# Kernel optimization log

Measured on AMD Instinct MI355X. Metric: run time of the kernel, lower is better.

The kernel has to match this reference:

```python
import jax, jax.numpy as jnp
import numpy as np

N_NODES = 100000
N_EDGES = 1600000
IN_DIM = 33
HID = 128
N_CLASSES = 10
N_GRAPHS = 128


def _glorot(key, shape):
    fan_in, fan_out = shape[0], shape[1]
    lim = (6.0 / (fan_in + fan_out)) ** 0.5
    return jax.random.uniform(key, shape, jnp.float32, -lim, lim)


def setup_inputs() -> dict:
    key = jax.random.key(0)
    ks = jax.random.split(key, 20)
    x = jax.random.normal(ks[0], (N_NODES, IN_DIM), jnp.float32)
    edge_index = jax.random.randint(ks[1], (2, N_EDGES), 0, N_NODES, jnp.int64)
    edge_w = jax.random.uniform(ks[2], (N_EDGES,), jnp.float32)
    batch = jnp.sort(jax.random.randint(ks[3], (N_NODES,), 0, N_GRAPHS, jnp.int64))
    p = {
        "We": _glorot(ks[4], (IN_DIM, HID)), "be": jnp.zeros((HID,), jnp.float32),
        "W1": _glorot(ks[5], (HID, HID)), "b1": jnp.zeros((HID,), jnp.float32),
        "W2": _glorot(ks[6], (HID, HID)), "b2": jnp.zeros((HID,), jnp.float32),
        "W3": _glorot(ks[7], (HID, HID)), "b3": jnp.zeros((HID,), jnp.float32),
        "W4": _glorot(ks[8], (HID, HID)), "b4": jnp.zeros((HID,), jnp.float32),
        "Wr1": _glorot(ks[9], (HID, HID // 2)), "br1": jnp.zeros((HID // 2,), jnp.float32),
        "Wr2": _glorot(ks[10], (HID // 2, HID // 4)), "br2": jnp.zeros((HID // 4,), jnp.float32),
        "Wr3": _glorot(ks[11], (HID // 4, N_CLASSES)),
    }
    return dict(x=x, edge_index=edge_index, edge_w=edge_w, batch=batch, **p)


def reference(x, edge_index, edge_w, batch,
              We, be, W1, b1, W2, b2, W3, b3, W4, b4,
              Wr1, br1, Wr2, br2, Wr3):
    N = x.shape[0]
    row, col = edge_index[0], edge_index[1]
    # PyG gcn_norm with add_self_loops=True: append (i,i) edges with weight 1
    loop = jnp.arange(N)
    row2 = jnp.concatenate([row, loop])
    col2 = jnp.concatenate([col, loop])
    w2 = jnp.concatenate([edge_w, jnp.ones((N,), edge_w.dtype)])
    deg = jax.ops.segment_sum(w2, col2, num_segments=N)  # in-degree incl. self-loop
    dinv = jnp.where(deg > 0, deg ** -0.5, 0.0)
    norm = dinv[row2] * w2 * dinv[col2]  # [E+N] symmetric normalization

    def conv(h, W, b):
        h = h @ W  # linear transform first (PyG GCNConv)
        msg = norm[:, None] * h[row2]  # gather + scale
        return jax.ops.segment_sum(msg, col2, num_segments=N) + b  # scatter-add to targets

    h = x @ We + be
    h = jax.nn.relu(conv(h, W1, b1))
    h = jax.nn.relu(conv(h, W2, b2))
    h = jax.nn.relu(conv(h, W3, b3))
    h = jax.nn.relu(conv(h, W4, b4))

    # global mean pool over graphs
    sums = jax.ops.segment_sum(h, batch, num_segments=N_GRAPHS)
    cnt = jax.ops.segment_sum(jnp.ones((N,), h.dtype), batch, num_segments=N_GRAPHS)
    pooled = sums / jnp.maximum(cnt, 1.0)[:, None]  # [G, HID]

    r = jax.nn.relu(pooled @ Wr1 + br1)
    r = jax.nn.relu(r @ Wr2 + br2)
    return r @ Wr3  # [G, n_classes]
```

## Files before the change

### kernel.cpp

```cpp
#include <hip/hip_runtime.h>
#include <hip/hip_bf16.h>

#define NN 100000
#define NE 1600000
#define IN_DIM 33
#define HID 128
#define NG 128
#define NCLS 10

using short8 = __attribute__((ext_vector_type(8))) short;
using floatx4 = __attribute__((ext_vector_type(4))) float;

static __device__ __forceinline__ size_t szmul(int a, int b) {
    return (size_t)a * (size_t)b;
}

static __device__ __forceinline__ unsigned short f2bf(float f) {
    unsigned u = __float_as_uint(f);
    u += 0x7fffu + ((u >> 16) & 1u);
    return (unsigned short)(u >> 16);
}
static __device__ __forceinline__ float bf_lo(unsigned u) { return __uint_as_float(u << 16); }
static __device__ __forceinline__ float bf_hi(unsigned u) { return __uint_as_float(u & 0xffff0000u); }

__global__ void k_init(int* bucket_cnt, int* bucket_fill, float* gsum) {
    int i = blockIdx.x * blockDim.x + threadIdx.x;
    if (i < 513) { bucket_cnt[i] = 0; bucket_fill[i] = 0; }
    if (i < NG * HID) gsum[i] = 0.0f;
}


__global__ __launch_bounds__(256) void k_bhist(const int* __restrict__ col,
                                               int* __restrict__ bucket_cnt, int e, int nbk) {
    __shared__ int hist[512];
    int tid = threadIdx.x;
    for (int i = tid; i < nbk; i += 256) hist[i] = 0;
    __syncthreads();
    for (int i = blockIdx.x * 256 + tid; i < e; i += 256 * 256)
        atomicAdd(&hist[col[i] >> 8], 1);
    __syncthreads();
    for (int i = tid; i < nbk; i += 256)
        if (hist[i]) atomicAdd(&bucket_cnt[i], hist[i]);
}

__global__ void k_scan_small(int* data, int nb) {
    __shared__ int s[512];
    int t = threadIdx.x;
    int v = (t < nb) ? data[t] : 0;
    s[t] = v;
    __syncthreads();
    for (int o = 1; o < 512; o <<= 1) {
        int a = (t >= o) ? s[t - o] : 0;
        __syncthreads();
        s[t] += a;
        __syncthreads();
    }
    if (t < nb) data[t] = s[t] - v;
    if (t == nb - 1) data[nb] = s[t];
}

__global__ __launch_bounds__(256) void k_bin_scatter(const int* __restrict__ row,
                                                     const int* __restrict__ col,
                                                     const float* __restrict__ w,
                                                     const int* __restrict__ bucket_base,
                                                     int* __restrict__ bucket_fill,
                                                     uint2* __restrict__ binned, int e, int nbk) {
    __shared__ int hist[512], rnk[512], basub[512];
    int tid = threadIdx.x;
    int c0 = blockIdx.x * 2048;
    for (int i = tid; i < nbk; i += 256) { hist[i] = 0; rnk[i] = 0; }
    __syncthreads();
    int myb[8]; unsigned myp[8]; unsigned myw[8];
#pragma unroll
    for (int u = 0; u < 8; ++u) {
        int idx = c0 + u * 256 + tid;
        int b = -1;
        if (idx < e) {
            int c = col[idx];
            int r = row[idx];
            myw[u] = __float_as_uint(w[idx]);
            b = c >> 8;
            myp[u] = ((unsigned)(c & 255) << 17) | (unsigned)r;
            atomicAdd(&hist[b], 1);
        }
        myb[u] = b;
    }
    __syncthreads();
    for (int i = tid; i < nbk; i += 256) {
        int c = hist[i];
        basub[i] = (c > 0) ? (bucket_base[i] + atomicAdd(&bucket_fill[i], c)) : 0;
    }
    __syncthreads();
#pragma unroll
    for (int u = 0; u < 8; ++u) {
        int b = myb[u];
        if (b >= 0) {
            int rk = atomicAdd(&rnk[b], 1);
            binned[basub[b] + rk] = make_uint2(myp[u], myw[u]);
        }
    }
}

__global__ __launch_bounds__(256) void k_bucket_cnt(const uint2* __restrict__ binned,
                                                    const int* __restrict__ bucket_base,
                                                    int* __restrict__ cnt, int n) {
    __shared__ int c256[256];
    int b = blockIdx.x, tid = threadIdx.x;
    c256[tid] = 0;
    __syncthreads();
    int beg = bucket_base[b], end = bucket_base[b + 1];
    for (int e2 = beg + tid; e2 < end; e2 += 256)
        atomicAdd(&c256[(binned[e2].x >> 17) & 255], 1);
    __syncthreads();
    int node = b * 256 + tid;
    if (node < n) cnt[node] = c256[tid];
}

#define SCAN_B 1024
__global__ void k_scan1(const int* __restrict__ cnt, int* __restrict__ rowptr,
                        int* __restrict__ bsums, int n) {
    __shared__ int s[SCAN_B];
    int t = threadIdx.x;
    int i = blockIdx.x * SCAN_B + t;
    int v = (i < n) ? cnt[i] : 0;
    s[t] = v;
    __syncthreads();
    for (int o = 1; o < SCAN_B; o <<= 1) {
        int a = (t >= o) ? s[t - o] : 0;
        __syncthreads();
        s[t] += a;
        __syncthreads();
    }
    if (i < n) rowptr[i] = s[t] - v;
    if (t == SCAN_B - 1) bsums[blockIdx.x] = s[t];
}

__global__ void k_scan3(int* rowptr, const int* __restrict__ bsums, int n, int etot) {
    int i = blockIdx.x * blockDim.x + threadIdx.x;
    if (i < n) rowptr[i] += bsums[i >> 10];
    else if (i == n) rowptr[n] = etot;
}

__global__ __launch_bounds__(256) void k_bucket_scatter(const uint2* __restrict__ binned,
                                                        const int* __restrict__ bucket_base,
                                                        const int* __restrict__ rowptr,
                                                        int2* __restrict__ csr, int n) {
    __shared__ int f256[256];
    int b = blockIdx.x, tid = threadIdx.x;
    f256[tid] = 0;
    __syncthreads();
    int beg = bucket_base[b], end = bucket_base[b + 1];
    for (int e2 = beg + tid; e2 < end; e2 += 256) {
        uint2 rec = binned[e2];
        int lo = (rec.x >> 17) & 255;
        int node = (b << 8) | lo;
        int src = rec.x & 0x1FFFF;
        int pos = rowptr[node] + atomicAdd(&f256[lo], 1);
        csr[pos] = make_int2(src, (int)rec.y);
    }
    (void)n;
}

__global__ void k_deg(const int* __restrict__ rowptr, const int2* __restrict__ csr,
                      float* __restrict__ dinv, float* __restrict__ selfn, int n) {
    int i = blockIdx.x * blockDim.x + threadIdx.x;
    if (i >= n) return;
    int beg = rowptr[i], end = rowptr[i + 1];
    float d = 1.0f;
    for (int e = beg; e < end; ++e) d += __int_as_float(csr[e].y);
    float di = (d > 0.0f) ? (1.0f / sqrtf(d)) : 0.0f;
    dinv[i] = di;
    selfn[i] = di * di;
}

__global__ void k_norm(const int* __restrict__ rowptr, int2* __restrict__ csr,
                       const float* __restrict__ dinv, int n) {
    int i = blockIdx.x * blockDim.x + threadIdx.x;
    if (i >= n) return;
    float dc = dinv[i];
    int beg = rowptr[i], end = rowptr[i + 1];
    for (int e = beg; e < end; ++e) {
        int2 v = csr[e];
        float nw = dinv[v.x] * __int_as_float(v.y) * dc;
        csr[e] = make_int2(v.x, __float_as_int(nw));
    }
}

__global__ void k_combine(const float* __restrict__ We, const float* __restrict__ W1,
                          const float* __restrict__ be,
                          float* __restrict__ M, float* __restrict__ v) {
    int f = threadIdx.x;
    int k = blockIdx.x;
    if (k < IN_DIM) {
        float a = 0.0f;
#pragma unroll 8
        for (int j = 0; j < HID; ++j) a += We[k * HID + j] * W1[j * HID + f];
        M[k * HID + f] = a;
    } else {
        float a = 0.0f;
#pragma unroll 8
        for (int j = 0; j < HID; ++j) a += be[j] * W1[j * HID + f];
        v[f] = a;
    }
}

__global__ void k_wcast3(const float* __restrict__ W1, const float* __restrict__ W2,
                         const float* __restrict__ W3, unsigned short* __restrict__ Wt) {
    int k = blockIdx.x, c = threadIdx.x, l = blockIdx.y;
    const float* W = (l == 0) ? W1 : (l == 1) ? W2 : W3;
    Wt[((size_t)l * HID + c) * HID + k] = f2bf(W[k * HID + c]);
}

__global__ __launch_bounds__(256) void k_gemm_x(const float* __restrict__ x,
                                                const float* __restrict__ M,
                                                const float* __restrict__ v,
                                                unsigned short* __restrict__ tb, int n) {
    __shared__ float sX[32 * IN_DIM];
    int n0 = blockIdx.x * 32;
    int tid = threadIdx.x;
    int cnt = n - n0; if (cnt > 32) cnt = 32;
    for (int idx = tid; idx < cnt * IN_DIM; idx += 256)
        sX[idx] = x[szmul(n0, IN_DIM) + idx];
    __syncthreads();
    int f = tid & 127, g = tid >> 7;
    float Mc[IN_DIM];
#pragma unroll
    for (int k = 0; k < IN_DIM; ++k) Mc[k] = M[k * HID + f];
    float vf = v[f];
    int ndEnd = g * 16 + 16; if (ndEnd > cnt) ndEnd = cnt;
    for (int nd = g * 16; nd < ndEnd; ++nd) {
        float a = vf;
#pragma unroll
        for (int k = 0; k < IN_DIM; ++k) a += sX[nd * IN_DIM + k] * Mc[k];
        tb[szmul(n0 + nd, HID) + f] = f2bf(a);
    }
}

__global__ __launch_bounds__(256) void k_gemm_mfma(const unsigned short* __restrict__ A,
                                                   const unsigned short* __restrict__ Wt,
                                                   unsigned short* __restrict__ T, int n) {
    int wave = threadIdx.x >> 6;
    int lane = threadIdx.x & 63;
    int r = lane & 15, kg = lane >> 4;
    int row0 = blockIdx.x * 64 + wave * 16;
    int arow = row0 + r;
    short8 af[4];
#pragma unroll
    for (int kk = 0; kk < 4; ++kk) {
        if (arow < n)
            af[kk] = *reinterpret_cast<const short8*>(A + szmul(arow, HID) + kk * 32 + kg * 8);
        else
            af[kk] = short8{0, 0, 0, 0, 0, 0, 0, 0};
    }
#pragma unroll
    for (int ct = 0; ct < 8; ++ct) {
        floatx4 acc = {0.f, 0.f, 0.f, 0.f};
#pragma unroll
        for (int kk = 0; kk < 4; ++kk) {
            short8 bf = *reinterpret_cast<const short8*>(
                Wt + (size_t)(ct * 16 + r) * HID + kk * 32 + kg * 8);
            acc = __builtin_amdgcn_mfma_f32_16x16x32_bf16(af[kk], bf, acc, 0, 0, 0);
        }
#pragma unroll
        for (int reg = 0; reg < 4; ++reg) {
            int orow = row0 + kg * 4 + reg;
            if (orow < n)
                T[szmul(orow, HID) + ct * 16 + r] = f2bf(acc[reg]);
        }
    }
}

__global__ __launch_bounds__(256) void k_aggregate(const uint4* __restrict__ tb,
                                                   const int* __restrict__ rowptr,
                                                   const int2* __restrict__ csr,
                                                   const float* __restrict__ selfn,
                                                   const float* __restrict__ bias,
                                                   uint4* __restrict__ hout, int n) {
    int i = (blockIdx.x * 256 + threadIdx.x) >> 6;
    if (i >= n) return;
    int lane = threadIdx.x & 63;
    int quarter = lane >> 4;
    int p = lane & 15;
    float a0 = 0.f, a1 = 0.f, a2 = 0.f, a3 = 0.f;
    float a4 = 0.f, a5 = 0.f, a6 = 0.f, a7 = 0.f;
    if (quarter == 0) {
        uint4 sv = tb[szmul(i, 16) + p];
        float sn = selfn[i];
        const float4* bp = reinterpret_cast<const float4*>(bias + p * 8);
        float4 b0 = bp[0], b1 = bp[1];
        a0 = b0.x + sn * bf_lo(sv.x); a1 = b0.y + sn * bf_hi(sv.x);
        a2 = b0.z + sn * bf_lo(sv.y); a3 = b0.w + sn * bf_hi(sv.y);
        a4 = b1.x + sn * bf_lo(sv.z); a5 = b1.y + sn * bf_hi(sv.z);
        a6 = b1.z + sn * bf_lo(sv.w); a7 = b1.w + sn * bf_hi(sv.w);
    }
    int beg = rowptr[i], end = rowptr[i + 1];
    for (int base = beg; base < end; base += 64) {
        int m = end - base; if (m > 64) m = 64;
        int2 e = make_int2(0, 0);
        if (lane < m) e = csr[base + lane];
#pragma unroll 2
        for (int j = 0; j < m; j += 4) {
            int jj = j + quarter;
            int src = __shfl(e.x, jj);
            float wj = __int_as_float(__shfl(e.y, jj));
            uint4 r = tb[szmul(src, 16) + p];
            a0 += wj * bf_lo(r.x); a1 += wj * bf_hi(r.x);
            a2 += wj * bf_lo(r.y); a3 += wj * bf_hi(r.y);
            a4 += wj * bf_lo(r.z); a5 += wj * bf_hi(r.z);
            a6 += wj * bf_lo(r.w); a7 += wj * bf_hi(r.w);
        }
    }
    a0 += __shfl_xor(a0, 16); a1 += __shfl_xor(a1, 16);
    a2 += __shfl_xor(a2, 16); a3 += __shfl_xor(a3, 16);
    a4 += __shfl_xor(a4, 16); a5 += __shfl_xor(a5, 16);
    a6 += __shfl_xor(a6, 16); a7 += __shfl_xor(a7, 16);
    a0 += __shfl_xor(a0, 32); a1 += __shfl_xor(a1, 32);
    a2 += __shfl_xor(a2, 32); a3 += __shfl_xor(a3, 32);
    a4 += __shfl_xor(a4, 32); a5 += __shfl_xor(a5, 32);
    a6 += __shfl_xor(a6, 32); a7 += __shfl_xor(a7, 32);
    if (quarter == 0) {
        unsigned u0 = (unsigned)f2bf(fmaxf(a0, 0.f)) | ((unsigned)f2bf(fmaxf(a1, 0.f)) << 16);
        unsigned u1 = (unsigned)f2bf(fmaxf(a2, 0.f)) | ((unsigned)f2bf(fmaxf(a3, 0.f)) << 16);
        unsigned u2 = (unsigned)f2bf(fmaxf(a4, 0.f)) | ((unsigned)f2bf(fmaxf(a5, 0.f)) << 16);
        unsigned u3 = (unsigned)f2bf(fmaxf(a6, 0.f)) | ((unsigned)f2bf(fmaxf(a7, 0.f)) << 16);
        hout[szmul(i, 16) + p] = make_uint4(u0, u1, u2, u3);
    }
}

__global__ void k_gcount_bs(const int* __restrict__ batch, int* gcnt, int n) {
    int g = threadIdx.x;
    if (g >= NG) return;
    int lo = 0, hi = n;
    while (lo < hi) { int mid = (lo + hi) >> 1; if (batch[mid] < g) lo = mid + 1; else hi = mid; }
    int start = lo;
    lo = 0; hi = n;
    while (lo < hi) { int mid = (lo + hi) >> 1; if (batch[mid] < g + 1) lo = mid + 1; else hi = mid; }
    gcnt[g] = lo - start;
}

__global__ __launch_bounds__(128) void k_pool(const unsigned short* __restrict__ h,
                                              const int* __restrict__ batch,
                                              float* gsum, int n) {
    int f = threadIdx.x;
    int i0 = blockIdx.x * 32;
    int i1 = min(i0 + 32, n);
    if (i0 >= n) return;
    float acc = 0.0f;
    int cur = batch[i0];
    for (int i = i0; i < i1; ++i) {
        int g = batch[i];
        if (g != cur) { atomicAdd(&gsum[cur * HID + f], acc); acc = 0.0f; cur = g; }
        acc += __uint_as_float((unsigned)h[szmul(i, HID) + f] << 16);
    }
    atomicAdd(&gsum[cur * HID + f], acc);
}

__global__ __launch_bounds__(128) void k_mlp(const float* __restrict__ gsum,
                                             const int* __restrict__ gcnt,
                                             const float* __restrict__ Wr1, const float* __restrict__ br1,
                                             const float* __restrict__ Wr2, const float* __restrict__ br2,
                                             const float* __restrict__ Wr3,
                                             float* __restrict__ out) {
    int g = blockIdx.x;
    int t = threadIdx.x;
    __shared__ float p[HID];
    __shared__ float r1[64];
    __shared__ float r2[32];
    float c = fmaxf((float)gcnt[g], 1.0f);
    p[t] = gsum[g * HID + t] / c;
    __syncthreads();
    if (t < 64) {
        float a = br1[t];
#pragma unroll 8
        for (int k = 0; k < HID; ++k) a += p[k] * Wr1[k * 64 + t];
        r1[t] = fmaxf(a, 0.0f);
    }
    __syncthreads();
    if (t < 32) {
        float a = br2[t];
#pragma unroll 8
        for (int k = 0; k < 64; ++k) a += r1[k] * Wr2[k * 32 + t];
        r2[t] = fmaxf(a, 0.0f);
    }
    __syncthreads();
    if (t < NCLS) {
        float a = 0.0f;
#pragma unroll
        for (int k = 0; k < 32; ++k) a += r2[k] * Wr3[k * NCLS + t];
        out[g * NCLS + t] = a;
    }
}

extern "C" void kernel_launch(void* const* d_in, const int* in_sizes, int n_in,
                              void* d_out, int out_size, void* d_ws, size_t ws_size,
                              hipStream_t stream) {
    const float* x     = (const float*)d_in[0];
    const int*   ei    = (const int*)d_in[1];
    const float* ew    = (const float*)d_in[2];
    const int*   batch = (const int*)d_in[3];
    const float* We  = (const float*)d_in[4];
    const float* be  = (const float*)d_in[5];
    const float* Wl[4] = { (const float*)d_in[6], (const float*)d_in[8],
                           (const float*)d_in[10], (const float*)d_in[12] };
    const float* bl[4] = { (const float*)d_in[7], (const float*)d_in[9],
                           (const float*)d_in[11], (const float*)d_in[13] };
    const float* Wr1 = (const float*)d_in[14];
    const float* br1 = (const float*)d_in[15];
    const float* Wr2 = (const float*)d_in[16];
    const float* br2 = (const float*)d_in[17];
    const float* Wr3 = (const float*)d_in[18];
    float* out = (float*)d_out;

    const int N = in_sizes[3];
    const int E = in_sizes[2];
    const int* row = ei;
    const int* col = ei + E;
    const int nbk = (N + 255) >> 8;

    char* w = (char*)d_ws;
    size_t off = 0;
    auto alloc = [&](size_t bytes) -> void* {
        void* p = w + off;
        off = (off + bytes + 255) & ~(size_t)255;
        return p;
    };
    float* dinv       = (float*)alloc((size_t)N * 4);
    float* selfn      = (float*)alloc((size_t)N * 4);
    int*   cnt        = (int*)  alloc((size_t)N * 4);
    int*   rowptr     = (int*)  alloc((size_t)(N + 1) * 4);
    int*   bsums      = (int*)  alloc(4096);
    int*   bucket_cnt = (int*)  alloc(513 * 4);
    int*   bucket_fill= (int*)  alloc(513 * 4);
    int2*  csr        = (int2*) alloc((size_t)E * 8);
    unsigned short* h  = (unsigned short*)alloc((size_t)N * HID * 2);
    unsigned short* tb = (unsigned short*)alloc((size_t)N * HID * 2);
    unsigned short* Wt = (unsigned short*)alloc((size_t)3 * HID * HID * 2);
    float* M          = (float*)alloc((size_t)IN_DIM * HID * 4);
    float* vbe        = (float*)alloc((size_t)HID * 4);
    float* gsum       = (float*)alloc((size_t)NG * HID * 4);
    int*   gcnt       = (int*)  alloc((size_t)NG * 4);
    uint2* binned     = (uint2*)tb;
    (void)ws_size;

    auto cdiv = [](int a, int b) { return (a + b - 1) / b; };

    k_init<<<64, 256, 0, stream>>>(bucket_cnt, bucket_fill, gsum);
    k_bhist<<<256, 256, 0, stream>>>(col, bucket_cnt, E, nbk);
    k_scan_small<<<1, 512, 0, stream>>>(bucket_cnt, nbk);
    k_bin_scatter<<<cdiv(E, 2048), 256, 0, stream>>>(row, col, ew, bucket_cnt,
                                                     bucket_fill, binned, E, nbk);
    k_bucket_cnt<<<nbk, 256, 0, stream>>>(binned, bucket_cnt, cnt, N);

    int nb = cdiv(N, SCAN_B);
    k_scan1<<<nb, SCAN_B, 0, stream>>>(cnt, rowptr, bsums, N);
    k_scan_small<<<1, 512, 0, stream>>>(bsums, nb);
    k_scan3<<<cdiv(N + 1, 256), 256, 0, stream>>>(rowptr, bsums, N, E);
    k_bucket_scatter<<<nbk, 256, 0, stream>>>(binned, bucket_cnt, rowptr, csr, N);

    k_deg<<<cdiv(N, 256), 256, 0, stream>>>(rowptr, csr, dinv, selfn, N);
    k_norm<<<cdiv(N, 256), 256, 0, stream>>>(rowptr, csr, dinv, N);

    k_combine<<<IN_DIM + 1, HID, 0, stream>>>(We, Wl[0], be, M, vbe);
    k_wcast3<<<dim3(HID, 3), HID, 0, stream>>>(Wl[1], Wl[2], Wl[3], Wt);

    k_gemm_x<<<cdiv(N, 32), 256, 0, stream>>>(x, M, vbe, tb, N);
    k_aggregate<<<cdiv(N, 4), 256, 0, stream>>>((const uint4*)tb, rowptr, csr,
                                                selfn, bl[0], (uint4*)h, N);

    for (int l = 1; l < 4; ++l) {
        k_gemm_mfma<<<cdiv(N, 64), 256, 0, stream>>>(h, Wt + (size_t)(l - 1) * HID * HID,
                                                     tb, N);
        k_aggregate<<<cdiv(N, 4), 256, 0, stream>>>((const uint4*)tb, rowptr, csr,
                                                    selfn, bl[l], (uint4*)h, N);
    }

    k_gcount_bs<<<1, 128, 0, stream>>>(batch, gcnt, N);
    k_pool<<<cdiv(N, 32), 128, 0, stream>>>(h, batch, gsum, N);
    k_mlp<<<NG, HID, 0, stream>>>(gsum, gcnt, Wr1, br1, Wr2, br2, Wr3, out);

    (void)out_size; (void)n_in;
}
```

Measured before the change: 538.7 us.

## Assign one 16-lane group per node in aggregation and double bin-scatter chunk

The aggregation kernel now gives each node a 16-thread group instead of a full 64-lane wavefront split into quarters. This removes the cooperative CSR load, the shuffles and the cross-quarter reduction, and packs four nodes per wavefront. Each group now walks its edge list serially with unroll 4 and reads the csr entries itself, so there is less memory-level parallelism per node and nodes of different degree within a wavefront can diverge. Separately, the bin-scatter kernel processes 4096 edges per block instead of 2048, which halves the global atomic traffic on bucket counters at the cost of more registers.

```diff
diff --git a/kernel.cpp b/kernel.cpp
--- a/kernel.cpp
+++ b/kernel.cpp
@@ -67,12 +67,12 @@
                                                      uint2* __restrict__ binned, int e, int nbk) {
     __shared__ int hist[512], rnk[512], basub[512];
     int tid = threadIdx.x;
-    int c0 = blockIdx.x * 2048;
+    int c0 = blockIdx.x * 4096;
     for (int i = tid; i < nbk; i += 256) { hist[i] = 0; rnk[i] = 0; }
     __syncthreads();
-    int myb[8]; unsigned myp[8]; unsigned myw[8];
-#pragma unroll
-    for (int u = 0; u < 8; ++u) {
+    int myb[16]; unsigned myp[16]; unsigned myw[16];
+#pragma unroll
+    for (int u = 0; u < 16; ++u) {
         int idx = c0 + u * 256 + tid;
         int b = -1;
         if (idx < e) {
@@ -92,7 +92,7 @@
     }
     __syncthreads();
 #pragma unroll
-    for (int u = 0; u < 8; ++u) {
+    for (int u = 0; u < 16; ++u) {
         int b = myb[u];
         if (b >= 0) {
             int rk = atomicAdd(&rnk[b], 1);
@@ -276,55 +276,33 @@
                                                    const float* __restrict__ selfn,
                                                    const float* __restrict__ bias,
                                                    uint4* __restrict__ hout, int n) {
-    int i = (blockIdx.x * 256 + threadIdx.x) >> 6;
+    int i = (blockIdx.x * 256 + threadIdx.x) >> 4;
     if (i >= n) return;
-    int lane = threadIdx.x & 63;
-    int quarter = lane >> 4;
-    int p = lane & 15;
-    float a0 = 0.f, a1 = 0.f, a2 = 0.f, a3 = 0.f;
-    float a4 = 0.f, a5 = 0.f, a6 = 0.f, a7 = 0.f;
-    if (quarter == 0) {
-        uint4 sv = tb[szmul(i, 16) + p];
-        float sn = selfn[i];
-        const float4* bp = reinterpret_cast<const float4*>(bias + p * 8);
-        float4 b0 = bp[0], b1 = bp[1];
-        a0 = b0.x + sn * bf_lo(sv.x); a1 = b0.y + sn * bf_hi(sv.x);
-        a2 = b0.z + sn * bf_lo(sv.y); a3 = b0.w + sn * bf_hi(sv.y);
-        a4 = b1.x + sn * bf_lo(sv.z); a5 = b1.y + sn * bf_hi(sv.z);
-        a6 = b1.z + sn * bf_lo(sv.w); a7 = b1.w + sn * bf_hi(sv.w);
-    }
+    int p = threadIdx.x & 15;
+    uint4 sv = tb[szmul(i, 16) + p];
+    float sn = selfn[i];
+    const float4* bp = reinterpret_cast<const float4*>(bias + p * 8);
+    float4 b0 = bp[0], b1 = bp[1];
+    float a0 = b0.x + sn * bf_lo(sv.x), a1 = b0.y + sn * bf_hi(sv.x);
+    float a2 = b0.z + sn * bf_lo(sv.y), a3 = b0.w + sn * bf_hi(sv.y);
+    float a4 = b1.x + sn * bf_lo(sv.z), a5 = b1.y + sn * bf_hi(sv.z);
+    float a6 = b1.z + sn * bf_lo(sv.w), a7 = b1.w + sn * bf_hi(sv.w);
     int beg = rowptr[i], end = rowptr[i + 1];
-    for (int base = beg; base < end; base += 64) {
-        int m = end - base; if (m > 64) m = 64;
-        int2 e = make_int2(0, 0);
-        if (lane < m) e = csr[base + lane];
-#pragma unroll 2
-        for (int j = 0; j < m; j += 4) {
-            int jj = j + quarter;
-            int src = __shfl(e.x, jj);
-            float wj = __int_as_float(__shfl(e.y, jj));
-            uint4 r = tb[szmul(src, 16) + p];
-            a0 += wj * bf_lo(r.x); a1 += wj * bf_hi(r.x);
-            a2 += wj * bf_lo(r.y); a3 += wj * bf_hi(r.y);
-            a4 += wj * bf_lo(r.z); a5 += wj * bf_hi(r.z);
-            a6 += wj * bf_lo(r.w); a7 += wj * bf_hi(r.w);
-        }
-    }
-    a0 += __shfl_xor(a0, 16); a1 += __shfl_xor(a1, 16);
-    a2 += __shfl_xor(a2, 16); a3 += __shfl_xor(a3, 16);
-    a4 += __shfl_xor(a4, 16); a5 += __shfl_xor(a5, 16);
-    a6 += __shfl_xor(a6, 16); a7 += __shfl_xor(a7, 16);
-    a0 += __shfl_xor(a0, 32); a1 += __shfl_xor(a1, 32);
-    a2 += __shfl_xor(a2, 32); a3 += __shfl_xor(a3, 32);
-    a4 += __shfl_xor(a4, 32); a5 += __shfl_xor(a5, 32);
-    a6 += __shfl_xor(a6, 32); a7 += __shfl_xor(a7, 32);
-    if (quarter == 0) {
-        unsigned u0 = (unsigned)f2bf(fmaxf(a0, 0.f)) | ((unsigned)f2bf(fmaxf(a1, 0.f)) << 16);
-        unsigned u1 = (unsigned)f2bf(fmaxf(a2, 0.f)) | ((unsigned)f2bf(fmaxf(a3, 0.f)) << 16);
-        unsigned u2 = (unsigned)f2bf(fmaxf(a4, 0.f)) | ((unsigned)f2bf(fmaxf(a5, 0.f)) << 16);
-        unsigned u3 = (unsigned)f2bf(fmaxf(a6, 0.f)) | ((unsigned)f2bf(fmaxf(a7, 0.f)) << 16);
-        hout[szmul(i, 16) + p] = make_uint4(u0, u1, u2, u3);
-    }
+#pragma unroll 4
+    for (int j = beg; j < end; ++j) {
+        int2 e = csr[j];
+        float wj = __int_as_float(e.y);
+        uint4 r = tb[szmul(e.x, 16) + p];
+        a0 += wj * bf_lo(r.x); a1 += wj * bf_hi(r.x);
+        a2 += wj * bf_lo(r.y); a3 += wj * bf_hi(r.y);
+        a4 += wj * bf_lo(r.z); a5 += wj * bf_hi(r.z);
+        a6 += wj * bf_lo(r.w); a7 += wj * bf_hi(r.w);
+    }
+    unsigned u0 = (unsigned)f2bf(fmaxf(a0, 0.f)) | ((unsigned)f2bf(fmaxf(a1, 0.f)) << 16);
+    unsigned u1 = (unsigned)f2bf(fmaxf(a2, 0.f)) | ((unsigned)f2bf(fmaxf(a3, 0.f)) << 16);
+    unsigned u2 = (unsigned)f2bf(fmaxf(a4, 0.f)) | ((unsigned)f2bf(fmaxf(a5, 0.f)) << 16);
+    unsigned u3 = (unsigned)f2bf(fmaxf(a6, 0.f)) | ((unsigned)f2bf(fmaxf(a7, 0.f)) << 16);
+    hout[szmul(i, 16) + p] = make_uint4(u0, u1, u2, u3);
 }
 
 __global__ void k_gcount_bs(const int* __restrict__ batch, int* gcnt, int n) {
@@ -447,7 +425,7 @@
     k_init<<<64, 256, 0, stream>>>(bucket_cnt, bucket_fill, gsum);
     k_bhist<<<256, 256, 0, stream>>>(col, bucket_cnt, E, nbk);
     k_scan_small<<<1, 512, 0, stream>>>(bucket_cnt, nbk);
-    k_bin_scatter<<<cdiv(E, 2048), 256, 0, stream>>>(row, col, ew, bucket_cnt,
+    k_bin_scatter<<<cdiv(E, 4096), 256, 0, stream>>>(row, col, ew, bucket_cnt,
                                                      bucket_fill, binned, E, nbk);
     k_bucket_cnt<<<nbk, 256, 0, stream>>>(binned, bucket_cnt, cnt, N);
 
@@ -464,14 +442,14 @@
     k_wcast3<<<dim3(HID, 3), HID, 0, stream>>>(Wl[1], Wl[2], Wl[3], Wt);
 
     k_gemm_x<<<cdiv(N, 32), 256, 0, stream>>>(x, M, vbe, tb, N);
-    k_aggregate<<<cdiv(N, 4), 256, 0, stream>>>((const uint4*)tb, rowptr, csr,
-                                                selfn, bl[0], (uint4*)h, N);
+    k_aggregate<<<cdiv(N, 16), 256, 0, stream>>>((const uint4*)tb, rowptr, csr,
+                                                 selfn, bl[0], (uint4*)h, N);
 
     for (int l = 1; l < 4; ++l) {
         k_gemm_mfma<<<cdiv(N, 64), 256, 0, stream>>>(h, Wt + (size_t)(l - 1) * HID * HID,
                                                      tb, N);
-        k_aggregate<<<cdiv(N, 4), 256, 0, stream>>>((const uint4*)tb, rowptr, csr,
-                                                    selfn, bl[l], (uint4*)h, N);
+        k_aggregate<<<cdiv(N, 16), 256, 0, stream>>>((const uint4*)tb, rowptr, csr,
+                                                     selfn, bl[l], (uint4*)h, N);
     }
 
     k_gcount_bs<<<1, 128, 0, stream>>>(batch, gcnt, N);
```

Result: faster. 514.2 us (-4.5%).
